# Kernel optimization log

Hardware: AMD Instinct MI355X
Metric: run time of the kernel (lower is better)

Reference implementation:

```python
import jax, jax.numpy as jnp
import numpy as np

B, S, DIM = 2, 1024, 4096
H, QLORA, KVLORA = 32, 1536, 512
NOPE, ROPE, VD = 128, 64, 128
QK_HEAD = NOPE + ROPE
SCALE = QK_HEAD ** -0.5
EPS = 1e-6
NEG = -1e9


def rms_norm(x, w):
    xf = x.astype(jnp.float32)
    y = xf * jax.lax.rsqrt(jnp.mean(xf * xf, axis=-1, keepdims=True) + EPS)
    return (y * w).astype(x.dtype)


def apply_rope(x, fc):
    # x: [b, s, h, r] with interleaved complex pairs; fc: [s, r//2, 2] = (cos, sin)
    b, s, h, r = x.shape
    xr = x.reshape(b, s, h, r // 2, 2)
    xe, xo = xr[..., 0], xr[..., 1]
    cos = fc[None, :, None, :, 0]
    sin = fc[None, :, None, :, 1]
    oe = xe * cos - xo * sin
    oo = xe * sin + xo * cos
    return jnp.stack([oe, oo], axis=-1).reshape(b, s, h, r)


def setup_inputs() -> dict:
    key = jax.random.key(0)
    ks = jax.random.split(key, 8)
    x = jax.random.normal(ks[0], (B, S, DIM), dtype=jnp.float32)
    pos = jnp.arange(S, dtype=jnp.float32)
    inv_freq = 1.0 / (10000.0 ** (jnp.arange(0, ROPE, 2, dtype=jnp.float32) / ROPE))
    ang = pos[:, None] * inv_freq[None, :]  # [S, ROPE//2]
    freqs_cis = jnp.stack([jnp.cos(ang), jnp.sin(ang)], axis=-1)  # [S, ROPE//2, 2]
    mask = jnp.triu(jnp.full((S, S), NEG, dtype=jnp.float32), k=1)
    def w(k, shape, fan_in):
        return jax.random.normal(k, shape, dtype=jnp.float32) * (fan_in ** -0.5)
    return {
        "x": x,
        "freqs_cis": freqs_cis,
        "mask": mask,
        "wq_a": w(ks[1], (DIM, QLORA), DIM),
        "q_norm_w": jnp.ones((QLORA,), jnp.float32),
        "wq_b": w(ks[2], (QLORA, H * QK_HEAD), QLORA),
        "wkv_a": w(ks[3], (DIM, KVLORA + ROPE), DIM),
        "kv_norm_w": jnp.ones((KVLORA,), jnp.float32),
        "wkv_b": w(ks[4], (H, NOPE + VD, KVLORA), KVLORA),
        "wo": w(ks[5], (H * VD, DIM), H * VD),
        "start_pos": 0,
    }


def reference(x, freqs_cis, mask, wq_a, q_norm_w, wq_b, wkv_a, kv_norm_w, wkv_b, wo, start_pos):
    bsz, seqlen, _ = x.shape
    # low-rank Q projection: wq_b(q_norm(wq_a(x)))
    q = rms_norm(x @ wq_a, q_norm_w) @ wq_b
    q = q.reshape(bsz, seqlen, H, QK_HEAD)
    q_nope, q_pe = q[..., :NOPE], q[..., NOPE:]
    q_pe = apply_rope(q_pe, freqs_cis)
    # compressed KV latent + shared rope key
    kv = x @ wkv_a
    c_kv, k_pe = kv[..., :KVLORA], kv[..., KVLORA:]
    k_pe = apply_rope(k_pe[:, :, None, :], freqs_cis)[:, :, 0, :]  # [b, t, ROPE]
    # weight absorption: q_nope @ wkv_b[:, :NOPE]  -> latent space
    q_abs = jnp.einsum('bshd,hdc->bshc', q_nope, wkv_b[:, :NOPE])  # [b,s,h,KVLORA]
    kv_n = rms_norm(c_kv, kv_norm_w)  # kv_cache[:bsz, :end_pos] (start_pos==0 prefill)
    scores = (jnp.einsum('bshc,btc->bsht', q_abs, kv_n)
              + jnp.einsum('bshr,btr->bsht', q_pe, k_pe)) * SCALE
    scores = scores + mask[None, :, None, :]
    probs = jax.nn.softmax(scores.astype(jnp.float32), axis=-1).astype(x.dtype)
    out = jnp.einsum('bsht,btc->bshc', probs, kv_n)
    out = jnp.einsum('bshc,hdc->bshd', out, wkv_b[:, -VD:])  # [b,s,h,VD]
    out = out.reshape(bsz, seqlen, H * VD) @ wo
    return out
```

## Files before the change

### kernel.cpp

```cpp
#include <hip/hip_runtime.h>
#include <stdint.h>

typedef unsigned short u16;
typedef uint32_t u32;
typedef short bf16x8 __attribute__((ext_vector_type(8)));
typedef float f32x4 __attribute__((ext_vector_type(4)));

#define DEV_INLINE __device__ __forceinline__

DEV_INLINE float b2f(u16 u) { union { u32 u; float f; } a; a.u = ((u32)u) << 16; return a.f; }
DEV_INLINE u16 f2b(float f) {
    union { float f; u32 u; } a; a.f = f;
    u32 u = a.u;
    u += 0x7fffu + ((u >> 16) & 1u);
    return (u16)(u >> 16);
}

typedef __attribute__((address_space(1))) u32 as1_u32;
typedef __attribute__((address_space(3))) u32 as3_u32;
DEV_INLINE void async16(void* lds, const void* g) {
    __builtin_amdgcn_global_load_lds((as1_u32*)g, (as3_u32*)lds, 16, 0, 0);
}

template <int MODE, bool CMASK = false, bool KCAP = false, bool SWZ = false, bool RSC = false>
__global__ __launch_bounds__(256) void gemm_bt(
    const u16* __restrict__ Ab, const u16* __restrict__ Bb, void* __restrict__ Cv,
    int K, long lda, long ldb, long ldc,
    long zA1, long zA2, long zB1, long zB2, long zC1, long zC2,
    float scale, const float* __restrict__ rowinv)
{
    __shared__ __align__(16) u16 As[2][128 * 32];
    __shared__ __align__(16) u16 Bs[2][128 * 32];

    int bx = blockIdx.x, by = blockIdx.y, bz = blockIdx.z;
    if (SWZ) {
        const int gx = gridDim.x, gy = gridDim.y;
        const int nwg = gx * gy * (int)gridDim.z;
        const int lin = bx + gx * (by + gy * bz);
        const int q = nwg >> 3, r = nwg & 7;
        const int xcd = lin & 7, idx = lin >> 3;
        const int wg = (xcd < r ? xcd * (q + 1) : r * (q + 1) + (xcd - r) * q) + idx;
        bx = wg % gx;
        const int t = wg / gx;
        by = t % gy;
        bz = t / gy;
    }

    const long row0 = (long)by * 128;
    const long col0 = (long)bx * 128;
    if (CMASK && col0 > row0) return;

    const long zb = bz >> 5, zh = bz & 31;
    const u16* A = Ab + zb * zA1 + zh * zA2;
    const u16* B = Bb + zb * zB1 + zh * zB2;

    const int tid = threadIdx.x;
    const int w = tid >> 6, l = tid & 63;
    const int quad = l >> 4, lrow = l & 15;
    const int wm = w & 1, wn = w >> 1;

    f32x4 acc[4][4];
#pragma unroll
    for (int mi = 0; mi < 4; mi++)
#pragma unroll
        for (int ni = 0; ni < 4; ni++) {
            f32x4 zv = {0.f, 0.f, 0.f, 0.f};
            acc[mi][ni] = zv;
        }

    const u16* gA = A + (row0 + w * 16 + (l >> 2)) * lda + (l & 3) * 8;
    const u16* gB = B + (col0 + w * 16 + (l >> 2)) * ldb + (l & 3) * 8;
    const int lofs = (w * 16) * 32;
    const long a64 = 64 * lda, b64 = 64 * ldb;

    int nk = K >> 5;
    if (KCAP) {
        const int nkc = (int)(row0 >> 5) + 4;
        nk = nk < nkc ? nk : nkc;
    }

    async16(&As[0][lofs], gA);
    async16(&As[0][lofs + 64 * 32], gA + a64);
    async16(&Bs[0][lofs], gB);
    async16(&Bs[0][lofs + 64 * 32], gB + b64);
    gA += 32;
    gB += 32;

    int cur = 0;
    for (int kt = 0; kt < nk; ++kt) {
        __syncthreads();
        if (kt + 1 < nk) {
            const int nxt = cur ^ 1;
            async16(&As[nxt][lofs], gA);
            async16(&As[nxt][lofs + 64 * 32], gA + a64);
            async16(&Bs[nxt][lofs], gB);
            async16(&Bs[nxt][lofs + 64 * 32], gB + b64);
            gA += 32;
            gB += 32;
        }
        bf16x8 af[4], bfr[4];
#pragma unroll
        for (int i = 0; i < 4; i++)
            af[i] = *(const bf16x8*)&As[cur][(wm * 64 + i * 16 + lrow) * 32 + quad * 8];
#pragma unroll
        for (int i = 0; i < 4; i++)
            bfr[i] = *(const bf16x8*)&Bs[cur][(wn * 64 + i * 16 + lrow) * 32 + quad * 8];
#pragma unroll
        for (int mi = 0; mi < 4; mi++)
#pragma unroll
            for (int ni = 0; ni < 4; ni++)
                acc[mi][ni] = __builtin_amdgcn_mfma_f32_16x16x32_bf16(af[mi], bfr[ni], acc[mi][ni], 0, 0, 0);
        cur ^= 1;
    }

    const long crow = row0 + wm * 64 + quad * 4;
    const long ccol = col0 + wn * 64 + lrow;
    float* Cf = (float*)Cv + zb * zC1 + zh * zC2;
    u16* Cb = (u16*)Cv + zb * zC1 + zh * zC2;
    const float lse = scale * 1.44269504088896f;
#pragma unroll
    for (int mi = 0; mi < 4; mi++)
#pragma unroll
        for (int rr = 0; rr < 4; rr++) {
            const long r = crow + mi * 16 + rr;
            float rs = 1.f;
            if (RSC) rs = rowinv[(long)bz * 1024 + r];
#pragma unroll
            for (int ni = 0; ni < 4; ni++) {
                const long c = ccol + ni * 16;
                const float v = acc[mi][ni][rr];
                if constexpr (MODE == 0) {
                    Cf[r * ldc + c] = v;
                } else if constexpr (MODE == 1) {
                    Cb[r * ldc + c] = f2b(RSC ? v * rs : v);
                } else {
                    const float arg = (c > r) ? -1e30f : v * lse;
                    Cb[r * ldc + c] = f2b(exp2f(arg));
                }
            }
        }
}

DEV_INLINE float ldval(const float* p) { return *p; }
DEV_INLINE float ldval(const u16* p) { return b2f(*p); }

template <typename SRC>
__global__ __launch_bounds__(256) void transpose_b16(
    const SRC* __restrict__ src, u16* __restrict__ dst,
    int R, int C, long ldS, long ldD, long zS, long zD)
{
    __shared__ float t[32][33];
    src += (long)blockIdx.z * zS;
    dst += (long)blockIdx.z * zD;
    const int tx = threadIdx.x & 31, ty = threadIdx.x >> 5;
    const long c0 = (long)blockIdx.x * 32, r0 = (long)blockIdx.y * 32;
#pragma unroll
    for (int i = 0; i < 4; i++) {
        long r = r0 + ty + i * 8, c = c0 + tx;
        if (r < R && c < C) t[ty + i * 8][tx] = ldval(&src[r * ldS + c]);
    }
    __syncthreads();
#pragma unroll
    for (int i = 0; i < 4; i++) {
        long c = c0 + ty + i * 8, r = r0 + tx;
        if (r < R && c < C) dst[c * ldD + r] = f2b(t[tx][ty + i * 8]);
    }
}

__global__ __launch_bounds__(256) void conv_b16(
    const float* __restrict__ src, u16* __restrict__ dst,
    int C, long ldS, long ldD, long zS, long zD)
{
    const long r = blockIdx.x;
    const float* s = src + (long)blockIdx.z * zS + r * ldS;
    u16* d = dst + (long)blockIdx.z * zD + r * ldD;
    for (int c = threadIdx.x; c < C; c += 256) d[c] = f2b(s[c]);
}

__global__ __launch_bounds__(256) void rmsnorm_b16(
    const float* __restrict__ X, const float* __restrict__ W, u16* __restrict__ Y,
    int C, long ldx, long ldy)
{
    const long r = blockIdx.x;
    const float* x = X + r * ldx;
    u16* y = Y + r * ldy;
    float ss = 0.f;
    for (int c = threadIdx.x; c < C; c += 256) { float v = x[c]; ss += v * v; }
    for (int off = 32; off; off >>= 1) ss += __shfl_down(ss, off);
    __shared__ float red[4];
    if ((threadIdx.x & 63) == 0) red[threadIdx.x >> 6] = ss;
    __syncthreads();
    const float tot = red[0] + red[1] + red[2] + red[3];
    const float inv = rsqrtf(tot / (float)C + 1e-6f);
    for (int c = threadIdx.x; c < C; c += 256) y[c] = f2b(x[c] * inv * W[c]);
}

__global__ __launch_bounds__(256) void rope_k_kernel(
    const float* __restrict__ kv, const float* __restrict__ fc, u16* __restrict__ kcat)
{
    const int idx = blockIdx.x * 256 + threadIdx.x;
    const int n = idx >> 5, i = idx & 31;
    const int s = n & 1023;
    const float e = kv[(long)n * 2176 + 2048 + 2 * i];
    const float o = kv[(long)n * 2176 + 2048 + 2 * i + 1];
    const float cs = fc[s * 64 + 2 * i], sn = fc[s * 64 + 2 * i + 1];
    kcat[(long)n * 576 + 512 + 2 * i] = f2b(e * cs - o * sn);
    kcat[(long)n * 576 + 512 + 2 * i + 1] = f2b(e * sn + o * cs);
}

__global__ __launch_bounds__(256) void rope_q_kernel(
    const u16* __restrict__ q, const float* __restrict__ fc, u16* __restrict__ qcat)
{
    const long idx = (long)blockIdx.x * 256 + threadIdx.x;
    const int i = (int)(idx & 31);
    const long nh = idx >> 5;
    const int h = (int)(nh & 31);
    const long n = nh >> 5;
    const int s = (int)(n & 1023);
    const float e = b2f(q[n * 6144 + h * 192 + 128 + 2 * i]);
    const float o = b2f(q[n * 6144 + h * 192 + 128 + 2 * i + 1]);
    const float cs = fc[s * 64 + 2 * i], sn = fc[s * 64 + 2 * i + 1];
    u16* dst = qcat + ((long)h * 2048 + n) * 576 + 512 + 2 * i;
    dst[0] = f2b(e * cs - o * sn);
    dst[1] = f2b(e * sn + o * cs);
}

__global__ __launch_bounds__(256) void rowsum_inv(
    const u16* __restrict__ P, float* __restrict__ inv)
{
    const int zt = blockIdx.y;
    const int row0 = blockIdx.x * 128;
    const int kcap = row0 + 128;
    const int t = threadIdx.x;
    const int r = t >> 1, half = t & 1;
    const u16* p = P + (long)zt * 1048576 + (long)(row0 + r) * 1024;
    float s = 0.f;
    for (int c = half * 8; c < kcap; c += 16) {
        bf16x8 v = *(const bf16x8*)&p[c];
#pragma unroll
        for (int j = 0; j < 8; j++) s += b2f((u16)v[j]);
    }
    s += __shfl_xor(s, 1);
    if (!half) inv[(long)zt * 1024 + row0 + r] = 1.0f / s;
}

__global__ void sentinel_kernel(float* out, float v) { out[0] = v; }

extern "C" void kernel_launch(void* const* d_in, const int* in_sizes, int n_in,
                              void* d_out, int out_size, void* d_ws, size_t ws_size,
                              hipStream_t stream)
{
    const float* x = (const float*)d_in[0];
    const float* fc = (const float*)d_in[1];
    const float* wq_a = (const float*)d_in[3];
    const float* qnw = (const float*)d_in[4];
    const float* wq_b = (const float*)d_in[5];
    const float* wkva = (const float*)d_in[6];
    const float* kvnw = (const float*)d_in[7];
    const float* wkvb = (const float*)d_in[8];
    const float* wo = (const float*)d_in[9];
    float* out = (float*)d_out;

    const size_t NEED = 252182528ULL;
    if (ws_size < NEED) {
        sentinel_kernel<<<1, 1, 0, stream>>>(out, (float)ws_size);
        return;
    }
    char* ws = (char*)d_ws;
    u16* wkbv   = (u16*)(ws + 0);
    u16* wo_t   = (u16*)(ws + 4194304);
    u16* kvn_t  = (u16*)(ws + 37748736);
    u16* kcat   = (u16*)(ws + 39845888);
    u16* qcat   = (u16*)(ws + 42205184);
    u16* o1     = (u16*)(ws + 42205184);
    u16* scores = (u16*)(ws + 117702656);
    u16*   xb     = (u16*)(ws + 117702656);
    u16*   wqkv_t = (u16*)(ws + 134479872);
    u16*   wq_b_t = (u16*)(ws + 152305664);
    u16*   wkbn_t = (u16*)(ws + 171180032);
    float* qk_lat = (float*)(ws + 175374336);
    u16*   qn     = (u16*)(ws + 193200128);
    u16*   q      = (u16*)(ws + 199491584);
    u16*   o2     = (u16*)(ws + 117702656);
    float* inv_g  = (float*)(ws + 251920384);

    const dim3 blk(256);
    const float SCALE = 0.0721687836487032f;

    transpose_b16<float><<<dim3(48, 128, 1), blk, 0, stream>>>(wq_a, wqkv_t, 4096, 1536, 1536, 4096, 0, 0);
    transpose_b16<float><<<dim3(18, 128, 1), blk, 0, stream>>>(wkva, wqkv_t + (long)1536 * 4096, 4096, 576, 576, 4096, 0, 0);
    transpose_b16<float><<<dim3(192, 48, 1), blk, 0, stream>>>(wq_b, wq_b_t, 1536, 6144, 6144, 1536, 0, 0);
    transpose_b16<float><<<dim3(16, 4, 32), blk, 0, stream>>>(wkvb, wkbn_t, 128, 512, 512, 128, 256 * 512, 512 * 128);
    conv_b16<<<dim3(128, 1, 32), blk, 0, stream>>>(wkvb + 128 * 512, wkbv, 512, 512, 512, 256 * 512, 128 * 512);
    transpose_b16<float><<<dim3(128, 128, 1), blk, 0, stream>>>(wo, wo_t, 4096, 4096, 4096, 4096, 0, 0);
    conv_b16<<<dim3(2048, 1, 1), blk, 0, stream>>>(x, xb, 4096, 4096, 4096, 0, 0);

    gemm_bt<0, false, false, true><<<dim3(17, 16, 1), blk, 0, stream>>>(
        xb, wqkv_t, qk_lat, 4096, 4096, 4096, 2176, 0, 0, 0, 0, 0, 0, 1.f, nullptr);
    rmsnorm_b16<<<2048, blk, 0, stream>>>(qk_lat, qnw, qn, 1536, 2176, 1536);
    rmsnorm_b16<<<2048, blk, 0, stream>>>(qk_lat + 1536, kvnw, kcat, 512, 2176, 576);
    rope_k_kernel<<<256, blk, 0, stream>>>(qk_lat, fc, kcat);
    transpose_b16<u16><<<dim3(16, 32, 2), blk, 0, stream>>>(kcat, kvn_t, 1024, 512, 576, 1024,
                                                            (long)1024 * 576, (long)512 * 1024);
    gemm_bt<1, false, false, true><<<dim3(48, 16, 1), blk, 0, stream>>>(
        qn, wq_b_t, q, 1536, 1536, 1536, 6144, 0, 0, 0, 0, 0, 0, 1.f, nullptr);
    gemm_bt<1, false, false, true><<<dim3(4, 16, 32), blk, 0, stream>>>(
        q, wkbn_t, qcat, 128, 6144, 128, 576,
        0, 192, 0, (long)512 * 128, 0, (long)2048 * 576, 1.f, nullptr);
    rope_q_kernel<<<8192, blk, 0, stream>>>(q, fc, qcat);
    gemm_bt<2, true, false, true><<<dim3(8, 8, 64), blk, 0, stream>>>(
        qcat, kcat, scores, 576, 576, 576, 1024,
        (long)1024 * 576, (long)2048 * 576, (long)1024 * 576, 0,
        (long)32 * 1048576, 1048576, SCALE, nullptr);
    rowsum_inv<<<dim3(8, 64), blk, 0, stream>>>(scores, inv_g);
    gemm_bt<1, false, true, true, true><<<dim3(4, 8, 64), blk, 0, stream>>>(
        scores, kvn_t, o1, 1024, 1024, 1024, 512,
        (long)32 * 1048576, 1048576, (long)512 * 1024, 0,
        (long)1024 * 512, (long)2048 * 512, 1.f, inv_g);
    gemm_bt<1, false, false, true><<<dim3(1, 16, 32), blk, 0, stream>>>(
        o1, wkbv, o2, 512, 512, 512, 4096,
        0, (long)2048 * 512, 0, (long)128 * 512, 0, 128, 1.f, nullptr);
    gemm_bt<0, false, false, true><<<dim3(32, 16, 1), blk, 0, stream>>>(
        o2, wo_t, out, 4096, 4096, 4096, 4096, 0, 0, 0, 0, 0, 0, 1.f, nullptr);
    (void)in_sizes; (void)n_in; (void)out_size; (void)d_in;
}
```

Before: 712.9 us.

## Add 4-stage async-LDS pipelined GEMM for wq_b and output projections

Adds a new gemm_pipe kernel with a four-buffer LDS ring. Tiles are loaded ahead with global_load_lds, synchronisation uses explicit vmcnt/lgkmcnt waits and sched barriers, and s_setprio is raised around the MFMA block. It replaces the double-buffered gemm_bt for the q up-projection and the final wo projection, aiming to hide global-memory latency behind compute. The deeper ring uses more LDS (64KB per block), which may reduce occupancy, and the kernel assumes K is at least 4 tiles and dimensions divisible by 128.

```diff
diff --git a/kernel.cpp b/kernel.cpp
--- a/kernel.cpp
+++ b/kernel.cpp
@@ -20,6 +20,128 @@
 typedef __attribute__((address_space(3))) u32 as3_u32;
 DEV_INLINE void async16(void* lds, const void* g) {
     __builtin_amdgcn_global_load_lds((as1_u32*)g, (as3_u32*)lds, 16, 0, 0);
+}
+
+#define GP_LGKM()                                         \
+    asm volatile("s_waitcnt lgkmcnt(0)" ::: "memory");    \
+    __builtin_amdgcn_sched_barrier(0)
+#define GP_VW(n)                                          \
+    asm volatile("s_waitcnt vmcnt(" #n ")" ::: "memory"); \
+    __builtin_amdgcn_sched_barrier(0)
+#define GP_BAR() __builtin_amdgcn_s_barrier()
+
+template <int MODE>
+__global__ __launch_bounds__(256, 2) void gemm_pipe(
+    const u16* __restrict__ A, const u16* __restrict__ B, void* __restrict__ Cv,
+    int K, long lda, long ldb, long ldc)
+{
+    __shared__ __align__(16) u16 As[4][128 * 32];
+    __shared__ __align__(16) u16 Bs[4][128 * 32];
+
+    int bx = blockIdx.x, by = blockIdx.y;
+    {
+        const int gx = gridDim.x, gy = gridDim.y;
+        const int nwg = gx * gy;
+        const int lin = bx + gx * by;
+        const int q = nwg >> 3, r = nwg & 7;
+        const int xcd = lin & 7, idx = lin >> 3;
+        const int wg = (xcd < r ? xcd * (q + 1) : r * (q + 1) + (xcd - r) * q) + idx;
+        bx = wg % gx;
+        by = wg / gx;
+    }
+    const long row0 = (long)by * 128, col0 = (long)bx * 128;
+
+    const int tid = threadIdx.x;
+    const int w = tid >> 6, l = tid & 63;
+    const int quad = l >> 4, lrow = l & 15;
+    const int wm = w & 1, wn = w >> 1;
+
+    f32x4 acc[4][4];
+#pragma unroll
+    for (int mi = 0; mi < 4; mi++)
+#pragma unroll
+        for (int ni = 0; ni < 4; ni++) {
+            f32x4 zv = {0.f, 0.f, 0.f, 0.f};
+            acc[mi][ni] = zv;
+        }
+
+    const int srow = tid >> 2;
+    const int schunk = (tid & 3) * 8;
+    const u16* gA = A + (row0 + srow) * lda + schunk;
+    const u16* gB = B + (col0 + srow) * ldb + schunk;
+    const long a64 = 64 * lda, b64 = 64 * ldb;
+
+#define PSTAGE(bi, kt) do {                                              \
+    const long ko_ = (long)(kt) * 32;                                    \
+    async16(&As[bi][srow * 32 + schunk], gA + ko_);                      \
+    async16(&As[bi][(64 + srow) * 32 + schunk], gA + a64 + ko_);         \
+    async16(&Bs[bi][srow * 32 + schunk], gB + ko_);                      \
+    async16(&Bs[bi][(64 + srow) * 32 + schunk], gB + b64 + ko_);         \
+} while (0)
+
+#define PCOMP(bi)                                                                     \
+    bf16x8 af[4], bfr[4];                                                             \
+    _Pragma("unroll") for (int i = 0; i < 4; i++)                                     \
+        af[i] = *(const bf16x8*)&As[bi][(wm * 64 + i * 16 + lrow) * 32 + quad * 8];   \
+    _Pragma("unroll") for (int i = 0; i < 4; i++)                                     \
+        bfr[i] = *(const bf16x8*)&Bs[bi][(wn * 64 + i * 16 + lrow) * 32 + quad * 8];  \
+    GP_LGKM();                                                                        \
+    __builtin_amdgcn_s_setprio(1);                                                    \
+    _Pragma("unroll") for (int mi = 0; mi < 4; mi++)                                  \
+    _Pragma("unroll") for (int ni = 0; ni < 4; ni++)                                  \
+        acc[mi][ni] = __builtin_amdgcn_mfma_f32_16x16x32_bf16(af[mi], bfr[ni], acc[mi][ni], 0, 0, 0); \
+    __builtin_amdgcn_s_setprio(0);
+
+    const int NT = K >> 5;
+
+    PSTAGE(0, 0);
+    PSTAGE(1, 1);
+    PSTAGE(2, 2);
+    GP_VW(8);
+    GP_BAR();
+
+    int t = 0;
+    for (; t + 3 < NT; ++t) {
+        PSTAGE((t + 3) & 3, t + 3);
+        { PCOMP(t & 3); }
+        GP_VW(8);
+        GP_BAR();
+    }
+    {
+        { PCOMP(t & 3); }
+        GP_VW(4);
+        GP_BAR();
+        ++t;
+    }
+    {
+        { PCOMP(t & 3); }
+        GP_VW(0);
+        GP_BAR();
+        ++t;
+    }
+    {
+        { PCOMP(t & 3); }
+    }
+#undef PSTAGE
+#undef PCOMP
+
+    const long crow = row0 + wm * 64 + quad * 4;
+    const long ccol = col0 + wn * 64 + lrow;
+    float* Cf = (float*)Cv;
+    u16* Cb = (u16*)Cv;
+#pragma unroll
+    for (int mi = 0; mi < 4; mi++)
+#pragma unroll
+        for (int rr = 0; rr < 4; rr++) {
+            const long r = crow + mi * 16 + rr;
+#pragma unroll
+            for (int ni = 0; ni < 4; ni++) {
+                const long c = ccol + ni * 16;
+                const float v = acc[mi][ni][rr];
+                if constexpr (MODE == 0) Cf[r * ldc + c] = v;
+                else Cb[r * ldc + c] = f2b(v);
+            }
+        }
 }
 
 template <int MODE, bool CMASK = false, bool KCAP = false, bool SWZ = false, bool RSC = false>
@@ -302,8 +424,7 @@
     rope_k_kernel<<<256, blk, 0, stream>>>(qk_lat, fc, kcat);
     transpose_b16<u16><<<dim3(16, 32, 2), blk, 0, stream>>>(kcat, kvn_t, 1024, 512, 576, 1024,
                                                             (long)1024 * 576, (long)512 * 1024);
-    gemm_bt<1, false, false, true><<<dim3(48, 16, 1), blk, 0, stream>>>(
-        qn, wq_b_t, q, 1536, 1536, 1536, 6144, 0, 0, 0, 0, 0, 0, 1.f, nullptr);
+    gemm_pipe<1><<<dim3(48, 16), blk, 0, stream>>>(qn, wq_b_t, q, 1536, 1536, 1536, 6144);
     gemm_bt<1, false, false, true><<<dim3(4, 16, 32), blk, 0, stream>>>(
         q, wkbn_t, qcat, 128, 6144, 128, 576,
         0, 192, 0, (long)512 * 128, 0, (long)2048 * 576, 1.f, nullptr);
@@ -320,7 +441,6 @@
     gemm_bt<1, false, false, true><<<dim3(1, 16, 32), blk, 0, stream>>>(
         o1, wkbv, o2, 512, 512, 512, 4096,
         0, (long)2048 * 512, 0, (long)128 * 512, 0, 128, 1.f, nullptr);
-    gemm_bt<0, false, false, true><<<dim3(32, 16, 1), blk, 0, stream>>>(
-        o2, wo_t, out, 4096, 4096, 4096, 4096, 0, 0, 0, 0, 0, 0, 1.f, nullptr);
+    gemm_pipe<0><<<dim3(32, 16), blk, 0, stream>>>(o2, wo_t, out, 4096, 4096, 4096, 4096);
     (void)in_sizes; (void)n_in; (void)out_size; (void)d_in;
 }
```

After: 731.4 us. 1.03x slower.
